# Kernel optimization log

Hardware: AMD Instinct MI355X
Metric: run time of the kernel (lower is better)

Reference implementation:

```python
import jax, jax.numpy as jnp
import numpy as np

TEMPERATURE = 1.0
N_NODES = 50000
N_EDGES = 1600000
BATCH = 2
C_IN = 64
C_OUT = 64


def setup_inputs() -> dict:
    key = jax.random.key(0)
    k = jax.random.split(key, 8)
    # edge_index with no self-loops: tgt = (src + 1 + off) % N, off in [0, N-2)
    src = jax.random.randint(k[0], (N_EDGES,), 0, N_NODES, dtype=jnp.int64)
    off = jax.random.randint(k[1], (N_EDGES,), 0, N_NODES - 1, dtype=jnp.int64)
    tgt = (src + 1 + off) % N_NODES
    edge_index = jnp.stack([src, tgt])  # (2, E)
    x = jax.random.normal(k[2], (BATCH, N_NODES, C_IN), dtype=jnp.float32)
    f_disc_orig = jax.random.uniform(k[3], (N_EDGES,), dtype=jnp.float32)
    fluxes = jax.random.normal(k[4], (BATCH, N_NODES), dtype=jnp.float32)
    W_conc = jax.random.normal(k[5], (C_OUT, C_IN), dtype=jnp.float32) * (1.0 / np.sqrt(C_IN))
    W_disc = jax.random.normal(k[6], (C_OUT, C_IN), dtype=jnp.float32) * (1.0 / np.sqrt(C_IN))
    bias = jnp.zeros((C_OUT,), dtype=jnp.float32)
    return {"x": x, "edge_index": edge_index, "f_disc_orig": f_disc_orig,
            "fluxes": fluxes, "W_conc": W_conc, "W_disc": W_disc, "bias": bias}


def reference(x, edge_index, f_disc_orig, fluxes, W_conc, W_disc, bias):
    B, N, _ = x.shape
    src0, tgt0 = edge_index[0], edge_index[1]  # original edges (no self-loops)
    loops = jnp.arange(N, dtype=edge_index.dtype)
    src = jnp.concatenate([src0, loops])  # (E+N,)
    tgt = jnp.concatenate([tgt0, loops])
    # GCN symmetric normalization D^{-1/2} A D^{-1/2} (with self-loops)
    deg = jnp.zeros((N,), x.dtype).at[tgt].add(1.0)
    dis = jnp.where(deg > 0, jax.lax.rsqrt(jnp.maximum(deg, 1e-30)), 0.0)
    norm = dis[src] * dis[tgt]  # (E+N,)
    # dynamic discordant strength on original (non-self-loop) edges
    sign_prod = jnp.tanh(fluxes[:, src0] * fluxes[:, tgt0] / TEMPERATURE)  # (B, E)
    keep = (1.0 + sign_prod) * 0.5
    fdo = f_disc_orig[None, :]
    f_disc = keep * fdo + (1.0 - keep) * (1.0 - fdo)  # (B, E)
    # self-loop messages are purely concordant (f_disc = 0)
    f_full = jnp.concatenate([f_disc, jnp.zeros((B, N), x.dtype)], axis=1)  # (B, E+N)
    # transform once per node, then gather per edge
    xc = jnp.einsum('bni,oi->bno', x, W_conc)  # (B, N, O)
    xd = jnp.einsum('bni,oi->bno', x, W_disc)
    msg = norm[None, :, None] * ((1.0 - f_full)[..., None] * xc[:, src] +
                                 f_full[..., None] * xd[:, src])  # (B, E+N, O)
    out = jnp.zeros((B, N, xc.shape[-1]), x.dtype).at[:, tgt].add(msg)
    return out + bias
```

## Files before the change

kernel.cpp:

```cpp
#include <hip/hip_runtime.h>
#include <math.h>


constexpr int C = 64;
constexpr int CNB = 128;
constexpr int CCAP = 5120;
constexpr int CHUNK = 4096;
constexpr int CPAD = 16;
constexpr int NCV = 1024;

typedef short short8 __attribute__((ext_vector_type(8)));
typedef float f32x4 __attribute__((ext_vector_type(4)));

__device__ __forceinline__ unsigned pack_bf16x2(float a, float b) {
    unsigned ua = __float_as_uint(a);
    ua = (ua + 0x7fffu + ((ua >> 16) & 1u)) >> 16;
    unsigned ub = __float_as_uint(b);
    ub = (ub + 0x7fffu + ((ub >> 16) & 1u)) >> 16;
    return ua | (ub << 16);
}
__device__ __forceinline__ float bflo(unsigned p) { return __uint_as_float(p << 16); }
__device__ __forceinline__ float bfhi(unsigned p) { return __uint_as_float(p & 0xffff0000u); }

__global__ __launch_bounds__(512) void hist_convert_kernel(
    const int* __restrict__ tgt, int* __restrict__ counts, int E, int nBin,
    const float* __restrict__ x, unsigned* __restrict__ xb2, int nwords) {
    const int tid = threadIdx.x;
    if (blockIdx.x >= nBin) {
        int gid = (blockIdx.x - nBin) * 512 + tid;
        const int stride = NCV * 512;
        const float2* x2 = (const float2*)x;
        for (int w = gid; w < nwords; w += stride) {
            float2 xv = x2[w];
            xb2[w] = pack_bf16x2(xv.x, xv.y);
        }
        return;
    }
    __shared__ int hcnt[512];
    const int chunk0 = blockIdx.x * CHUNK;
    hcnt[tid] = 0;
    __syncthreads();
#pragma unroll 4
    for (int k = 0; k < CHUNK / 512; ++k) {
        int e = chunk0 + tid + k * 512;
        if (e < E) atomicAdd(&hcnt[tgt[e] >> 7], 1);
    }
    __syncthreads();
    counts[blockIdx.x * 512 + tid] = hcnt[tid];
}

__global__ __launch_bounds__(512) void scanbases_kernel(
    const int* __restrict__ counts, int* __restrict__ bases,
    int* __restrict__ coarseCursor, int nBin) {
    const int c = blockIdx.x;
    const int tid = threadIdx.x;
    __shared__ int sc[512];
    int v = (tid < nBin) ? counts[tid * 512 + c] : 0;
    sc[tid] = v;
    __syncthreads();
    for (int off = 1; off < 512; off <<= 1) {
        int t = (tid >= off) ? sc[tid - off] : 0;
        __syncthreads();
        sc[tid] += t;
        __syncthreads();
    }
    if (tid < nBin) bases[tid * 512 + c] = sc[tid] - v;
    if (tid == 511) coarseCursor[c * CPAD] = sc[511];
}

__global__ __launch_bounds__(512) void scatter_kernel(
    const int* __restrict__ src, const int* __restrict__ tgt,
    const float* __restrict__ fdo, const int* __restrict__ bases,
    unsigned long long* __restrict__ slab, int E) {
    __shared__ int hcnt[512];
    __shared__ int hbase[512];
    const int tid = threadIdx.x;
    const int chunk0 = blockIdx.x * CHUNK;
    hcnt[tid] = 0;
    hbase[tid] = bases[blockIdx.x * 512 + tid];
    __syncthreads();
#pragma unroll 4
    for (int k = 0; k < CHUNK / 512; ++k) {
        int e = chunk0 + tid + k * 512;
        if (e < E) {
            int t = tgt[e];
            int b = t >> 7;
            int pos = hbase[b] + atomicAdd(&hcnt[b], 1);
            if (pos < CCAP) {
                unsigned q = (unsigned)(fdo[e] * 32767.0f + 0.5f);
                unsigned long long en = (unsigned long long)(unsigned)src[e]
                                      | ((unsigned long long)(unsigned)(t & 127) << 17)
                                      | ((unsigned long long)q << 24);
                slab[(size_t)b * CCAP + pos] = en;
            }
        }
    }
}

__global__ __launch_bounds__(512) void binA2_kernel(
    const unsigned long long* __restrict__ slab,
    const int* __restrict__ coarseCursor, const float* __restrict__ flux,
    unsigned* __restrict__ epackFine, float4* __restrict__ nodeinfo, int N) {
    const int b = blockIdx.x;
    const int tid = threadIdx.x;
    __shared__ unsigned eout[CCAP];
    __shared__ int ncnt[CNB];
    __shared__ int nbase[CNB];
    __shared__ int ncur[CNB];
    int cnt = min(coarseCursor[b << 4], CCAP);
    if (tid < CNB) { ncnt[tid] = 0; ncur[tid] = 0; }
    __syncthreads();
    const unsigned long long* sl = slab + (size_t)b * CCAP;
    for (int i = tid; i < cnt; i += 512)
        atomicAdd(&ncnt[(int)((sl[i] >> 17) & 127)], 1);
    __syncthreads();
    if (tid < 64) {
        int c0 = ncnt[2 * tid];
        int c1 = ncnt[2 * tid + 1];
        int s = c0 + c1;
        for (int off = 1; off < 64; off <<= 1) {
            int v = __shfl_up(s, off, 64);
            if (tid >= off) s += v;
        }
        nbase[2 * tid] = s - c1 - c0;
        nbase[2 * tid + 1] = s - c1;
    }
    __syncthreads();
    for (int i = tid; i < cnt; i += 512) {
        unsigned long long e = sl[i];
        int tl = (int)((e >> 17) & 127);
        int pos = nbase[tl] + atomicAdd(&ncur[tl], 1);
        eout[pos] = (unsigned)(e & 0x1FFFFull)
                  | ((unsigned)((e >> 24) & 0x7FFF) << 17);
    }
    if (tid < CNB) {
        int n = b * CNB + tid;
        if (n < N) {
            int dg = ncnt[tid];
            int rs = b * CCAP + nbase[tid];
            float4 ni;
            ni.x = rsqrtf((float)(dg + 1));
            ni.y = flux[n];
            ni.z = flux[N + n];
            ni.w = __int_as_float((dg << 21) | rs);
            nodeinfo[n] = ni;
        }
    }
    __syncthreads();
    unsigned* out = epackFine + (size_t)b * CCAP;
    for (int i = tid; i < cnt; i += 512) out[i] = eout[i];
}

__global__ __launch_bounds__(256) void aggregate_kernel(
    const float4* __restrict__ nodeinfo, const unsigned* __restrict__ epackFine,
    const unsigned* __restrict__ xb2, unsigned* __restrict__ up,
    unsigned* __restrict__ vp, int N) {
    const int lane = threadIdx.x & 63;
    const int wslot = threadIdx.x >> 6;
    const int node = blockIdx.x * 4 + wslot;
    __shared__ float4 s_e[4][2][64];
    if (node >= N) return;
    const int e2 = lane >> 4;
    const int q16 = lane & 15;
    const int g = q16 >> 3;
    const int p = q16 & 7;
    float4 ni = nodeinfo[node];
    const unsigned wbits = (unsigned)__float_as_int(ni.w);
    const int start = (int)(wbits & 0x1FFFFFu);
    const int end = start + (int)(wbits >> 21);
    const float dt = ni.x, f0t = ni.y, f1t = ni.z;
    const char* xbg = (const char*)xb2 + (size_t)g * N * 128 + p * 16;
    float au[8] = {0, 0, 0, 0, 0, 0, 0, 0};
    float av[8] = {0, 0, 0, 0, 0, 0, 0, 0};
    for (int base = start; base < end; base += 64) {
        int cnt = min(64, end - base);
        int cntp = (cnt + 7) & ~7;
        if (lane < cnt) {
            unsigned pe = epackFine[base + lane];
            int s = (int)(pe & 0x1FFFFu);
            float fd = (float)(pe >> 17) * (1.0f / 32767.0f);
            float4 nis = nodeinfo[s];
            float nrm = nis.x * dt;
            float p0 = nis.y * f0t;
            float p1 = nis.z * f1t;
            float k0 = 1.0f / (1.0f + __expf(-2.0f * p0));
            float k1 = 1.0f / (1.0f + __expf(-2.0f * p1));
            float w = 2.0f * fd - 1.0f;
            float f0 = fmaf(k0, w, 1.0f - fd);
            float f1 = fmaf(k1, w, 1.0f - fd);
            float soff = __int_as_float(s << 7);
            s_e[wslot][0][lane] = make_float4(soff, nrm * (1.0f - f0), nrm * f0, 0.f);
            s_e[wslot][1][lane] = make_float4(soff, nrm * (1.0f - f1), nrm * f1, 0.f);
        } else if (lane < cntp) {
            float4 z = make_float4(0.f, 0.f, 0.f, 0.f);
            s_e[wslot][0][lane] = z;
            s_e[wslot][1][lane] = z;
        }
        float4 rA = s_e[wslot][g][e2];
        float4 rB = s_e[wslot][g][4 + e2];
        uint4 xA = *(const uint4*)(xbg + __float_as_int(rA.x));
        uint4 xB = *(const uint4*)(xbg + __float_as_int(rB.x));
        for (int j = 8; j < cntp; j += 8) {
            float4 nA = s_e[wslot][g][j + e2];
            float4 nB = s_e[wslot][g][j + 4 + e2];
            uint4 pA = *(const uint4*)(xbg + __float_as_int(nA.x));
            uint4 pB = *(const uint4*)(xbg + __float_as_int(nB.x));
#pragma unroll
            for (int w = 0; w < 4; ++w) {
                unsigned xp = (&xA.x)[w];
                float lo = bflo(xp), hi = bfhi(xp);
                au[2 * w] = fmaf(rA.y, lo, au[2 * w]);
                au[2 * w + 1] = fmaf(rA.y, hi, au[2 * w + 1]);
                av[2 * w] = fmaf(rA.z, lo, av[2 * w]);
                av[2 * w + 1] = fmaf(rA.z, hi, av[2 * w + 1]);
                unsigned xq = (&xB.x)[w];
                float lo2 = bflo(xq), hi2 = bfhi(xq);
                au[2 * w] = fmaf(rB.y, lo2, au[2 * w]);
                au[2 * w + 1] = fmaf(rB.y, hi2, au[2 * w + 1]);
                av[2 * w] = fmaf(rB.z, lo2, av[2 * w]);
                av[2 * w + 1] = fmaf(rB.z, hi2, av[2 * w + 1]);
            }
            xA = pA; rA = nA;
            xB = pB; rB = nB;
        }
#pragma unroll
        for (int w = 0; w < 4; ++w) {
            unsigned xp = (&xA.x)[w];
            float lo = bflo(xp), hi = bfhi(xp);
            au[2 * w] = fmaf(rA.y, lo, au[2 * w]);
            au[2 * w + 1] = fmaf(rA.y, hi, au[2 * w + 1]);
            av[2 * w] = fmaf(rA.z, lo, av[2 * w]);
            av[2 * w + 1] = fmaf(rA.z, hi, av[2 * w + 1]);
            unsigned xq = (&xB.x)[w];
            float lo2 = bflo(xq), hi2 = bfhi(xq);
            au[2 * w] = fmaf(rB.y, lo2, au[2 * w]);
            au[2 * w + 1] = fmaf(rB.y, hi2, au[2 * w + 1]);
            av[2 * w] = fmaf(rB.z, lo2, av[2 * w]);
            av[2 * w + 1] = fmaf(rB.z, hi2, av[2 * w + 1]);
        }
    }
#pragma unroll
    for (int k = 0; k < 8; ++k) {
        au[k] += __shfl_xor(au[k], 16, 64);
        au[k] += __shfl_xor(au[k], 32, 64);
        av[k] += __shfl_xor(av[k], 16, 64);
        av[k] += __shfl_xor(av[k], 32, 64);
    }
    if (e2 == 0) {
        uint4 xs = *(const uint4*)(xbg + ((size_t)node << 7));
        float d2 = dt * dt;
#pragma unroll
        for (int w = 0; w < 4; ++w) {
            unsigned xp = (&xs.x)[w];
            au[2 * w] = fmaf(d2, bflo(xp), au[2 * w]);
            au[2 * w + 1] = fmaf(d2, bfhi(xp), au[2 * w + 1]);
        }
        uint4 uo, vo;
        uo.x = pack_bf16x2(au[0], au[1]);
        uo.y = pack_bf16x2(au[2], au[3]);
        uo.z = pack_bf16x2(au[4], au[5]);
        uo.w = pack_bf16x2(au[6], au[7]);
        vo.x = pack_bf16x2(av[0], av[1]);
        vo.y = pack_bf16x2(av[2], av[3]);
        vo.z = pack_bf16x2(av[4], av[5]);
        vo.w = pack_bf16x2(av[6], av[7]);
        size_t wo = ((size_t)(g * N + node)) * 32 + 4 * p;
        *(uint4*)(up + wo) = uo;
        *(uint4*)(vp + wo) = vo;
    }
}

__device__ __forceinline__ short8 make_bfrag(const float* __restrict__ row, int off) {
    const float4* p = (const float4*)(row + off);
    float4 lo = p[0], hi = p[1];
    uint4 w;
    w.x = pack_bf16x2(lo.x, lo.y);
    w.y = pack_bf16x2(lo.z, lo.w);
    w.z = pack_bf16x2(hi.x, hi.y);
    w.w = pack_bf16x2(hi.z, hi.w);
    return __builtin_bit_cast(short8, w);
}

__global__ __launch_bounds__(256) void gemm_mfma_kernel(
    const unsigned* __restrict__ up, const unsigned* __restrict__ vp,
    const float* __restrict__ Wc, const float* __restrict__ Wd,
    const float* __restrict__ bias, float* __restrict__ out, int ntiles) {
    const int lane = threadIdx.x & 63;
    const int nl = lane & 15;
    const int quad = lane >> 4;
    const int wave = blockIdx.x * 4 + (threadIdx.x >> 6);
    const int nwaves = gridDim.x * 4;

    short8 bf[4][4];
    float bt[4];
#pragma unroll
    for (int t = 0; t < 4; ++t) {
        int n = 16 * t + nl;
        const float* wcr = Wc + n * 64;
        const float* wdr = Wd + n * 64;
        bf[0][t] = make_bfrag(wcr, quad * 8);
        bf[1][t] = make_bfrag(wcr, 32 + quad * 8);
        bf[2][t] = make_bfrag(wdr, quad * 8);
        bf[3][t] = make_bfrag(wdr, 32 + quad * 8);
        bt[t] = bias[n];
    }

    for (int tile = wave; tile < ntiles; tile += nwaves) {
        int row = tile * 16 + nl;
        const uint4* ur = (const uint4*)(up + (size_t)row * 32);
        const uint4* vr = (const uint4*)(vp + (size_t)row * 32);
        short8 a0 = __builtin_bit_cast(short8, ur[quad]);
        short8 a1 = __builtin_bit_cast(short8, ur[4 + quad]);
        short8 a2 = __builtin_bit_cast(short8, vr[quad]);
        short8 a3 = __builtin_bit_cast(short8, vr[4 + quad]);
        f32x4 acc[4];
#pragma unroll
        for (int t = 0; t < 4; ++t) {
            f32x4 z = {0.f, 0.f, 0.f, 0.f};
            acc[t] = __builtin_amdgcn_mfma_f32_16x16x32_bf16(a0, bf[0][t], z, 0, 0, 0);
            acc[t] = __builtin_amdgcn_mfma_f32_16x16x32_bf16(a1, bf[1][t], acc[t], 0, 0, 0);
            acc[t] = __builtin_amdgcn_mfma_f32_16x16x32_bf16(a2, bf[2][t], acc[t], 0, 0, 0);
            acc[t] = __builtin_amdgcn_mfma_f32_16x16x32_bf16(a3, bf[3][t], acc[t], 0, 0, 0);
        }
        float* ob = out + ((size_t)(tile * 16 + quad * 4) << 6);
#pragma unroll
        for (int t = 0; t < 4; ++t) {
            int col = 16 * t + nl;
#pragma unroll
            for (int r = 0; r < 4; ++r)
                ob[(r << 6) + col] = acc[t][r] + bt[t];
        }
    }
}

extern "C" void kernel_launch(void* const* d_in, const int* in_sizes, int n_in,
                              void* d_out, int out_size, void* d_ws, size_t ws_size,
                              hipStream_t stream) {
    const float* x = (const float*)d_in[0];
    const int* ei = (const int*)d_in[1];
    const float* fdo = (const float*)d_in[2];
    const float* flux = (const float*)d_in[3];
    const float* Wc = (const float*)d_in[4];
    const float* Wd = (const float*)d_in[5];
    const float* bias = (const float*)d_in[6];
    float* out = (float*)d_out;

    const int E = in_sizes[2];
    const int BN = in_sizes[3];
    const int N = BN / 2;
    const int ncoarse = (N + CNB - 1) / CNB;
    const int nBin = (E + CHUNK - 1) / CHUNK;

    auto align = [](size_t o) { return (o + 255) & ~(size_t)255; };
    char* ws = (char*)d_ws;
    size_t o = 0;
    int* coarseCursor = (int*)(ws + o);            o = align(o + (size_t)ncoarse * CPAD * 4);
    float4* nodeinfo = (float4*)(ws + o);          o = align(o + (size_t)N * 16);
    unsigned long long* slab = (unsigned long long*)(ws + o);
    unsigned* up = (unsigned*)slab;
    o = align(o + (size_t)ncoarse * CCAP * 8);
    unsigned* epackFine = (unsigned*)(ws + o);     o = align(o + (size_t)ncoarse * CCAP * 4);
    unsigned* xb2 = (unsigned*)(ws + o);           o = align(o + (size_t)BN * 32 * 4);
    unsigned* vp = (unsigned*)(ws + o);            o = align(o + (size_t)BN * 32 * 4);
    int* counts = (int*)(ws + o);                  o = align(o + (size_t)nBin * 512 * 4);
    int* bases = (int*)(ws + o);                   o += (size_t)nBin * 512 * 4;

    const int* srcp = ei;
    const int* tgtp = ei + E;

    hist_convert_kernel<<<nBin + NCV, 512, 0, stream>>>(
        tgtp, counts, E, nBin, x, xb2, BN * 32);
    scanbases_kernel<<<ncoarse, 512, 0, stream>>>(counts, bases, coarseCursor, nBin);
    scatter_kernel<<<nBin, 512, 0, stream>>>(srcp, tgtp, fdo, bases, slab, E);
    binA2_kernel<<<ncoarse, 512, 0, stream>>>(slab, coarseCursor, flux,
                                              epackFine, nodeinfo, N);
    aggregate_kernel<<<(N + 3) / 4, 256, 0, stream>>>(nodeinfo, epackFine, xb2,
                                                      up, vp, N);
    gemm_mfma_kernel<<<512, 256, 0, stream>>>(up, vp, Wc, Wd, bias, out, BN / 16);
}
```

Baseline: 206.4 us.

## Halve edge chunk size, transpose count layout, move x conversion into scatter

```diff
diff --git a/kernel.cpp b/kernel.cpp
--- a/kernel.cpp
+++ b/kernel.cpp
@@ -5,7 +5,8 @@
 constexpr int C = 64;
 constexpr int CNB = 128;
 constexpr int CCAP = 5120;
-constexpr int CHUNK = 4096;
+constexpr int CHUNK = 2048;
+constexpr int NBP = 784;
 constexpr int CPAD = 16;
 constexpr int NCV = 1024;
 
@@ -22,8 +23,52 @@
 __device__ __forceinline__ float bflo(unsigned p) { return __uint_as_float(p << 16); }
 __device__ __forceinline__ float bfhi(unsigned p) { return __uint_as_float(p & 0xffff0000u); }
 
-__global__ __launch_bounds__(512) void hist_convert_kernel(
-    const int* __restrict__ tgt, int* __restrict__ counts, int E, int nBin,
+__global__ __launch_bounds__(512) void hist_kernel(
+    const int* __restrict__ tgt, int* __restrict__ counts, int E) {
+    __shared__ int hcnt[512];
+    const int tid = threadIdx.x;
+    const int chunk0 = blockIdx.x * CHUNK;
+    hcnt[tid] = 0;
+    __syncthreads();
+#pragma unroll 4
+    for (int k = 0; k < CHUNK / 512; ++k) {
+        int e = chunk0 + tid + k * 512;
+        if (e < E) atomicAdd(&hcnt[tgt[e] >> 7], 1);
+    }
+    __syncthreads();
+    counts[tid * NBP + blockIdx.x] = hcnt[tid];
+}
+
+__global__ __launch_bounds__(512) void scanbases_kernel(
+    const int* __restrict__ counts, int* __restrict__ bases,
+    int* __restrict__ coarseCursor, int nBin) {
+    const int c = blockIdx.x;
+    const int tid = threadIdx.x;
+    __shared__ int sc[512];
+    const int* row = counts + (size_t)c * NBP;
+    int a = 0, b = 0;
+    if (2 * tid < nBin) a = row[2 * tid];
+    if (2 * tid + 1 < nBin) b = row[2 * tid + 1];
+    int s = a + b;
+    sc[tid] = s;
+    __syncthreads();
+    for (int off = 1; off < 512; off <<= 1) {
+        int t = (tid >= off) ? sc[tid - off] : 0;
+        __syncthreads();
+        sc[tid] += t;
+        __syncthreads();
+    }
+    int excl = sc[tid] - s;
+    int* brow = bases + (size_t)c * NBP;
+    if (2 * tid < nBin) brow[2 * tid] = excl;
+    if (2 * tid + 1 < nBin) brow[2 * tid + 1] = excl + a;
+    if (tid == 511) coarseCursor[c * CPAD] = sc[511];
+}
+
+__global__ __launch_bounds__(512) void scatter_convert_kernel(
+    const int* __restrict__ src, const int* __restrict__ tgt,
+    const float* __restrict__ fdo, const int* __restrict__ bases,
+    unsigned long long* __restrict__ slab, int E, int nBin,
     const float* __restrict__ x, unsigned* __restrict__ xb2, int nwords) {
     const int tid = threadIdx.x;
     if (blockIdx.x >= nBin) {
@@ -37,47 +82,10 @@
         return;
     }
     __shared__ int hcnt[512];
+    __shared__ int hbase[512];
     const int chunk0 = blockIdx.x * CHUNK;
     hcnt[tid] = 0;
-    __syncthreads();
-#pragma unroll 4
-    for (int k = 0; k < CHUNK / 512; ++k) {
-        int e = chunk0 + tid + k * 512;
-        if (e < E) atomicAdd(&hcnt[tgt[e] >> 7], 1);
-    }
-    __syncthreads();
-    counts[blockIdx.x * 512 + tid] = hcnt[tid];
-}
-
-__global__ __launch_bounds__(512) void scanbases_kernel(
-    const int* __restrict__ counts, int* __restrict__ bases,
-    int* __restrict__ coarseCursor, int nBin) {
-    const int c = blockIdx.x;
-    const int tid = threadIdx.x;
-    __shared__ int sc[512];
-    int v = (tid < nBin) ? counts[tid * 512 + c] : 0;
-    sc[tid] = v;
-    __syncthreads();
-    for (int off = 1; off < 512; off <<= 1) {
-        int t = (tid >= off) ? sc[tid - off] : 0;
-        __syncthreads();
-        sc[tid] += t;
-        __syncthreads();
-    }
-    if (tid < nBin) bases[tid * 512 + c] = sc[tid] - v;
-    if (tid == 511) coarseCursor[c * CPAD] = sc[511];
-}
-
-__global__ __launch_bounds__(512) void scatter_kernel(
-    const int* __restrict__ src, const int* __restrict__ tgt,
-    const float* __restrict__ fdo, const int* __restrict__ bases,
-    unsigned long long* __restrict__ slab, int E) {
-    __shared__ int hcnt[512];
-    __shared__ int hbase[512];
-    const int tid = threadIdx.x;
-    const int chunk0 = blockIdx.x * CHUNK;
-    hcnt[tid] = 0;
-    hbase[tid] = bases[blockIdx.x * 512 + tid];
+    hbase[tid] = bases[(size_t)tid * NBP + blockIdx.x];
     __syncthreads();
 #pragma unroll 4
     for (int k = 0; k < CHUNK / 512; ++k) {
@@ -362,16 +370,16 @@
     unsigned* epackFine = (unsigned*)(ws + o);     o = align(o + (size_t)ncoarse * CCAP * 4);
     unsigned* xb2 = (unsigned*)(ws + o);           o = align(o + (size_t)BN * 32 * 4);
     unsigned* vp = (unsigned*)(ws + o);            o = align(o + (size_t)BN * 32 * 4);
-    int* counts = (int*)(ws + o);                  o = align(o + (size_t)nBin * 512 * 4);
-    int* bases = (int*)(ws + o);                   o += (size_t)nBin * 512 * 4;
+    int* counts = (int*)(ws + o);                  o = align(o + (size_t)512 * NBP * 4);
+    int* bases = (int*)(ws + o);                   o += (size_t)512 * NBP * 4;
 
     const int* srcp = ei;
     const int* tgtp = ei + E;
 
-    hist_convert_kernel<<<nBin + NCV, 512, 0, stream>>>(
-        tgtp, counts, E, nBin, x, xb2, BN * 32);
+    hist_kernel<<<nBin, 512, 0, stream>>>(tgtp, counts, E);
     scanbases_kernel<<<ncoarse, 512, 0, stream>>>(counts, bases, coarseCursor, nBin);
-    scatter_kernel<<<nBin, 512, 0, stream>>>(srcp, tgtp, fdo, bases, slab, E);
+    scatter_convert_kernel<<<nBin + NCV, 512, 0, stream>>>(
+        srcp, tgtp, fdo, bases, slab, E, nBin, x, xb2, BN * 32);
     binA2_kernel<<<ncoarse, 512, 0, stream>>>(slab, coarseCursor, flux,
                                               epackFine, nodeinfo, N);
     aggregate_kernel<<<(N + 3) / 4, 256, 0, stream>>>(nodeinfo, epackFine, xb2,
```

After: 205.6 us. No clear change (-0.4%).
